# Optimization experiments

Hardware: AMD Instinct MI355X
Metric: run time of the kernel (lower is better)

The kernel has to match this reference:

```python
import jax, jax.numpy as jnp
from jax import lax
import numpy as np

# Shapes / hyperparams (match init_kwargs and input_specs)
B, C1, H1, W1 = 4, 128, 128, 128      # x1: low-level feature map
C2, H2, W2 = 64, 64, 64               # x2: high-level feature map (H1 = rate*H2)
KSIZE, STRIDE, RATE, SIZE = 3, 1, 2, 2
KERNEL = SIZE * RATE                  # 4 = raw patch size
SCALE = 10.0
GROUPS, OUT_C = 4, 64
RATES = (1, 2, 4, 8)
L = H2 * W2                           # number of patches / attention bins


def extract_patches(x, k, s):
    """torch extract_patches: zero-pad (k-1)//2, unfold -> [B, L, C, k, k]."""
    pad = (k - 1) // 2 if k != 1 else 0
    p = lax.conv_general_dilated_patches(x, (k, k), (s, s), [(pad, pad), (pad, pad)])
    Bn, Ckk, oH, oW = p.shape
    C = Ckk // (k * k)
    p = p.reshape(Bn, C, k, k, oH, oW)
    return jnp.transpose(p, (0, 4, 5, 1, 2, 3)).reshape(Bn, oH * oW, C, k, k)


def setup_inputs():
    key = jax.random.key(0)
    ks = jax.random.split(key, 5)
    x1 = jax.random.normal(ks[0], (B, C1, H1, W1), jnp.float32)
    x2 = jax.random.normal(ks[1], (B, C2, H2, W2), jnp.float32)
    # mask: 1 indicates holes; central square hole at x1 resolution
    mask = jnp.zeros((B, 1, H1, W1), jnp.float32)
    mask = mask.at[:, :, H1 // 4:3 * H1 // 4, W1 // 4:3 * W1 // 4].set(1.0)
    mask_all = jax.random.uniform(ks[2], (B, 1, H2, W2), jnp.float32)
    conv_w = jax.random.normal(ks[3], (GROUPS, OUT_C // GROUPS, C1, 3, 3), jnp.float32) * 0.05
    conv_b = jax.random.normal(ks[4], (GROUPS, OUT_C // GROUPS), jnp.float32) * 0.01
    return {"x1": x1, "x2": x2, "mask": mask, "mask_all": mask_all,
            "conv_w": conv_w, "conv_b": conv_b}


def reference(x1, x2, mask, mask_all, conv_w, conv_b):
    raw_w = extract_patches(x1, KERNEL, RATE * STRIDE)   # [B, L, C1, 4, 4] value patches
    w = extract_patches(x2, KSIZE, STRIDE)               # [B, L, C2, 3, 3] key patches
    # F.interpolate(mask, size=x1 HW, align_corners=True) is identity (mask already H1xW1)
    m = extract_patches(mask, KERNEL, 2).mean(axis=(2, 3, 4))   # [B, L]
    mm = (m == 0.0).astype(x1.dtype)                            # 1 = fully valid patch
    # F.interpolate(mask_all, size=x2 HW) is identity (already H2xW2)

    pad_s = (KSIZE - 1) // 2
    pad_t = KERNEL - 1 - (KERNEL - 1) // 2  # conv_transpose2d(padding=(KERNEL-1)//2)

    def attend(xi, wi, raw_wi, mi, ma):
        # xi [C2,H2,W2], wi [L,C2,3,3], raw_wi [L,C1,4,4], mi [L], ma [1,H2,W2]
        norm = jnp.sqrt(jnp.sum(wi * wi, axis=(1, 2, 3), keepdims=True))
        wn = wi / jnp.maximum(norm, 1e-4)
        # correlation scores: conv2d(xi, normalized key patches) -> [L, H2, W2]
        yi = lax.conv_general_dilated(
            xi[None], wn, (1, 1), [(pad_s, pad_s)] * 2,
            dimension_numbers=('NCHW', 'OIHW', 'NCHW'))[0]
        mi3 = mi[:, None, None]
        yi = yi * mi3 * ma
        yi = jax.nn.softmax(yi * SCALE, axis=0)
        yi = jnp.maximum(yi * mi3 * ma, 1e-8)
        # value aggregation: conv_transpose2d(yi, raw_wi, stride=RATE, padding=1)
        out = lax.conv_general_dilated(
            yi[None], raw_wi[:, :, ::-1, ::-1], (1, 1), [(pad_t, pad_t)] * 2,
            lhs_dilation=(RATE, RATE),
            dimension_numbers=('NCHW', 'IOHW', 'NCHW'))[0]
        return out / float(KERNEL)                        # [C1, H1, W1]

    y = jax.vmap(attend)(x2, w, raw_w, mm, mask_all)      # [B, C1, H1, W1]

    # fuse: GROUPS dilated 3x3 conv + ReLU branches, concatenated on channels
    outs = []
    for i in range(GROUPS):
        r = RATES[i]
        o = lax.conv_general_dilated(
            y, conv_w[i], (1, 1), [(r, r)] * 2, rhs_dilation=(r, r),
            dimension_numbers=('NCHW', 'OIHW', 'NCHW'))
        outs.append(jax.nn.relu(o + conv_b[i][None, :, None, None]))
    return jnp.concatenate(outs, axis=1)                  # [B, OUT_C, H1, W1]
```

## Files before the change

### kernel.cpp

```cpp
#include <hip/hip_runtime.h>
#include <math.h>

typedef _Float16 f16;
typedef __attribute__((ext_vector_type(8))) _Float16 f16x8;
typedef __attribute__((ext_vector_type(4))) float f32x4;
typedef __attribute__((ext_vector_type(16))) float f32x16;

#define LPOS 4096
#define KPAT 576
#define RPAT 2048
#define PPAD 20736
#define ROWS 18432

#define GLDS(g, l) __builtin_amdgcn_global_load_lds( \
    (const __attribute__((address_space(1))) void*)(g), \
    (__attribute__((address_space(3))) void*)(l), 16, 0, 0)

__global__ __launch_bounds__(64) void build_P_norm(const float* __restrict__ x2b,
                                                   f16* __restrict__ Ph,
                                                   float* __restrict__ rnorm) {
    int pos = blockIdx.x;
    int u = pos >> 6, v = pos & 63;
    int tid = threadIdx.x;
    float ss = 0.f;
    for (int k = tid; k < KPAT; k += 64) {
        int c = k / 9, r9 = k % 9;
        int di = r9 / 3, dj = r9 % 3;
        int yy = u + di - 1, xx = v + dj - 1;
        float val = 0.f;
        if (yy >= 0 && yy < 64 && xx >= 0 && xx < 64)
            val = x2b[c * 4096 + yy * 64 + xx];
        Ph[pos * KPAT + k] = (f16)val;
        ss += val * val;
    }
#pragma unroll
    for (int off = 32; off; off >>= 1) ss += __shfl_xor(ss, off, 64);
    if (tid == 0) rnorm[pos] = 1.f / fmaxf(sqrtf(ss), 1e-4f);
}

__global__ __launch_bounds__(256) void compact_mask_all(const float* __restrict__ mask,
                                                        int* __restrict__ cidx_all,
                                                        int* __restrict__ nk_all) {
    int b = blockIdx.x;
    const float* maskb = mask + (size_t)b * 16384;
    int* cidx = cidx_all + b * 4352;
    int* nk = nk_all + b * 2;
    int tid = threadIdx.x;
    int keep[16];
    int cnt = 0;
#pragma unroll
    for (int e = 0; e < 16; ++e) {
        int pos = tid * 16 + e;
        int pu = pos >> 6, pv = pos & 63;
        float s = 0.f;
        for (int t = 0; t < 4; ++t)
            for (int w = 0; w < 4; ++w) {
                int yy = 2 * pu - 1 + t, xx = 2 * pv - 1 + w;
                if (yy >= 0 && yy < 128 && xx >= 0 && xx < 128)
                    s += maskb[yy * 128 + xx];
            }
        keep[e] = (s == 0.f) ? 1 : 0;
        cnt += keep[e];
    }
    __shared__ int ps[256];
    ps[tid] = cnt;
    __syncthreads();
    for (int off = 1; off < 256; off <<= 1) {
        int v = (tid >= off) ? ps[tid - off] : 0;
        __syncthreads();
        ps[tid] += v;
        __syncthreads();
    }
    int total = ps[255];
    int base = ps[tid] - cnt;
#pragma unroll
    for (int e = 0; e < 16; ++e)
        if (keep[e]) cidx[base++] = tid * 16 + e;
    for (int i = total + tid; i < 4352; i += 256) cidx[i] = 0;
    if (tid == 0) { nk[0] = total; nk[1] = (total + 63) & ~63; }
}

__global__ __launch_bounds__(256) void zero_halo(f16* __restrict__ ybTp) {
    int idx = blockIdx.x * 256 + threadIdx.x;
    int b = idx / 331776; if (b >= 4) return;
    int rem = idx % 331776;
    int q = rem & 15, pos = rem >> 4;
    int yy = pos / 144, xx = pos % 144;
    if (yy >= 8 && yy < 136 && xx >= 8 && xx < 136) return;
    *(f16x8*)(ybTp + (size_t)b * PPAD * 128 + (size_t)yy * ROWS + q * 1152 + xx * 8) = (f16x8){};
}

__global__ __launch_bounds__(256) void gemm_score_mfma(const f16* __restrict__ Ph,
                                                       const int* __restrict__ cidx,
                                                       const float* __restrict__ rnorm,
                                                       const int* __restrict__ nk,
                                                       f16* __restrict__ S) {
    int n0 = blockIdx.x * 128;
    if (n0 >= nk[0]) return;
    __shared__ f16 Ash[128 * 32], Bsh[128 * 32];
    int tid = threadIdx.x;
    int w = tid >> 6, lane = tid & 63;
    int wy = w >> 1, wx = w & 1;
    int m0 = blockIdx.y * 128;
    f32x16 acc[2][2];
#pragma unroll
    for (int mt = 0; mt < 2; ++mt)
#pragma unroll
        for (int nt = 0; nt < 2; ++nt)
#pragma unroll
            for (int e = 0; e < 16; ++e) acc[mt][nt][e] = 0.f;
    int srow = lane >> 2;
    int cblk = lane & 3;
    int scol = (cblk ^ ((srow >> 1) & 3)) * 8;
    int dcol = cblk * 8;
    int l31 = lane & 31, kh2 = lane >> 5;
    int arow[2], brow[2], asw[2], bsw[2];
#pragma unroll
    for (int i = 0; i < 2; ++i) {
        arow[i] = wy * 64 + i * 32 + l31;
        brow[i] = wx * 64 + i * 32 + l31;
        asw[i] = (arow[i] >> 1) & 3;
        bsw[i] = (brow[i] >> 1) & 3;
    }
    const f16* Asrc[2]; const f16* Bsrc[2]; int ldso[2];
#pragma unroll
    for (int i = 0; i < 2; ++i) {
        int row = w * 32 + i * 16 + srow;
        ldso[i] = row * 32 + dcol;
        Asrc[i] = Ph + (size_t)(m0 + row) * KPAT + scol;
        Bsrc[i] = Ph + (size_t)cidx[n0 + row] * KPAT + scol;
    }
    for (int k0 = 0; k0 < KPAT; k0 += 32) {
#pragma unroll
        for (int i = 0; i < 2; ++i) {
            GLDS(Asrc[i] + k0, Ash + ldso[i]);
            GLDS(Bsrc[i] + k0, Bsh + ldso[i]);
        }
        __syncthreads();
#pragma unroll
        for (int kh = 0; kh < 2; ++kh) {
            int blk = kh * 2 + kh2;
            f16x8 va[2], vb[2];
#pragma unroll
            for (int i = 0; i < 2; ++i) {
                va[i] = *(const f16x8*)&Ash[arow[i] * 32 + ((blk ^ asw[i]) * 8)];
                vb[i] = *(const f16x8*)&Bsh[brow[i] * 32 + ((blk ^ bsw[i]) * 8)];
            }
#pragma unroll
            for (int mt = 0; mt < 2; ++mt)
#pragma unroll
                for (int nt = 0; nt < 2; ++nt)
                    acc[mt][nt] = __builtin_amdgcn_mfma_f32_32x32x16_f16(va[mt], vb[nt], acc[mt][nt], 0, 0, 0);
        }
        __syncthreads();
    }
    int rbase = 4 * kh2;
#pragma unroll
    for (int mt = 0; mt < 2; ++mt)
#pragma unroll
        for (int nt = 0; nt < 2; ++nt) {
            int col = n0 + wx * 64 + nt * 32 + l31;
            float rn = rnorm[cidx[col]];
#pragma unroll
            for (int rg = 0; rg < 16; ++rg) {
                int row = m0 + wy * 64 + mt * 32 + (rg & 3) + 8 * (rg >> 2) + rbase;
                S[(size_t)row * LPOS + col] = (f16)(acc[mt][nt][rg] * rn);
            }
        }
}

__global__ __launch_bounds__(256) void softmax_mask(const f16* __restrict__ S,
                                                    const int* __restrict__ nk,
                                                    const float* __restrict__ mab,
                                                    f16* __restrict__ Ah) {
    int pos = blockIdx.x;
    int tid = threadIdx.x;
    int nkeep = nk[0], kpad = nk[1];
    float ma = mab[pos];
    float sc = 10.0f * ma;
    const f16* Srow = S + (size_t)pos * LPOS;
    float v[16];
    float vmax = (nkeep < LPOS) ? 0.f : -3.0e38f;
#pragma unroll
    for (int i = 0; i < 2; ++i) {
        int jb = (tid + i * 256) * 8;
        f16x8 x8 = *(const f16x8*)(Srow + jb);
#pragma unroll
        for (int e = 0; e < 8; ++e) {
            float x = (jb + e < nkeep) ? (float)x8[e] * sc : -3.0e38f;
            v[i * 8 + e] = x;
            vmax = fmaxf(vmax, x);
        }
    }
#pragma unroll
    for (int off = 32; off; off >>= 1) vmax = fmaxf(vmax, __shfl_xor(vmax, off, 64));
    __shared__ float sred[4];
    int wid = tid >> 6;
    if ((tid & 63) == 0) sred[wid] = vmax;
    __syncthreads();
    vmax = fmaxf(fmaxf(sred[0], sred[1]), fmaxf(sred[2], sred[3]));
    __syncthreads();
    float ssum = 0.f;
#pragma unroll
    for (int i = 0; i < 16; ++i) {
        float e = (v[i] > -1.0e37f) ? __expf(v[i] - vmax) : 0.f;
        v[i] = e;
        ssum += e;
    }
#pragma unroll
    for (int off = 32; off; off >>= 1) ssum += __shfl_xor(ssum, off, 64);
    if ((tid & 63) == 0) sred[wid] = ssum;
    __syncthreads();
    float total = sred[0] + sred[1] + sred[2] + sred[3]
                + (float)(LPOS - nkeep) * __expf(-vmax);
    float inv = 1.f / total;
#pragma unroll
    for (int i = 0; i < 2; ++i) {
        int jb = (tid + i * 256) * 8;
        if (jb >= kpad) continue;
        f16x8 h;
#pragma unroll
        for (int e = 0; e < 8; ++e)
            h[e] = (jb + e < nkeep) ? (f16)(v[i * 8 + e] * inv * ma) : (f16)0.f;
        *(f16x8*)(Ah + (size_t)pos * LPOS + jb) = h;
    }
}

__global__ __launch_bounds__(256) void build_Rt(const float* __restrict__ x1b,
                                                const int* __restrict__ cidx,
                                                const int* __restrict__ nk,
                                                f16* __restrict__ Rt) {
    int idx = blockIdx.x * 256 + threadIdx.x;
    int j = idx & 4095, n = idx >> 12;
    if (j >= nk[1]) return;
    int p = cidx[j];
    int pu = p >> 6, pv = p & 63;
    int t = (n >> 9) & 3, s = (n >> 7) & 3, c = n & 127;
    int yy = 2 * pu - 1 + t, xx = 2 * pv - 1 + s;
    float val = 0.f;
    if (yy >= 0 && yy < 128 && xx >= 0 && xx < 128)
        val = x1b[c * 16384 + yy * 128 + xx];
    Rt[idx] = (f16)val;
}

__global__ __launch_bounds__(256) void gemm_deconv_mfma(const f16* __restrict__ A,
                                                        const f16* __restrict__ Bt,
                                                        const int* __restrict__ nk,
                                                        f16* __restrict__ V) {
    __shared__ f16 Ash[128 * 64], Bsh[128 * 64];
    int kpad = nk[1];
    int id = blockIdx.x;
    int m0 = ((id & 7) * 4 + ((id >> 3) & 3)) * 128;
    int n0 = (id >> 5) * 128;
    int tid = threadIdx.x;
    int w = tid >> 6, lane = tid & 63;
    int wy = w >> 1, wx = w & 1;
    f32x16 acc[2][2];
#pragma unroll
    for (int mt = 0; mt < 2; ++mt)
#pragma unroll
        for (int nt = 0; nt < 2; ++nt)
#pragma unroll
            for (int e = 0; e < 16; ++e) acc[mt][nt][e] = 0.f;
    int srow = lane >> 3;
    int cblk = lane & 7;
    int scol = (cblk ^ srow) * 8;
    int l31 = lane & 31, kh2 = lane >> 5;
    int f7 = l31 & 7;
    int arow[2], brow[2];
#pragma unroll
    for (int i = 0; i < 2; ++i) {
        arow[i] = wy * 64 + i * 32 + l31;
        brow[i] = wx * 64 + i * 32 + l31;
    }
    for (int k0 = 0; k0 < kpad; k0 += 64) {
#pragma unroll
        for (int i = 0; i < 4; ++i) {
            int row = w * 32 + i * 8 + srow;
            int ldso = row * 64 + cblk * 8;
            GLDS(A + (size_t)(m0 + row) * LPOS + k0 + scol, Ash + ldso);
            GLDS(Bt + (size_t)(n0 + row) * LPOS + k0 + scol, Bsh + ldso);
        }
        __syncthreads();
#pragma unroll
        for (int kh = 0; kh < 4; ++kh) {
            int slot = (kh * 2 + kh2) ^ f7;
            f16x8 va[2], vb[2];
#pragma unroll
            for (int i = 0; i < 2; ++i) {
                va[i] = *(const f16x8*)&Ash[arow[i] * 64 + slot * 8];
                vb[i] = *(const f16x8*)&Bsh[brow[i] * 64 + slot * 8];
            }
#pragma unroll
            for (int mt = 0; mt < 2; ++mt)
#pragma unroll
                for (int nt = 0; nt < 2; ++nt)
                    acc[mt][nt] = __builtin_amdgcn_mfma_f32_32x32x16_f16(va[mt], vb[nt], acc[mt][nt], 0, 0, 0);
        }
        __syncthreads();
    }
    int rbase = 4 * kh2;
#pragma unroll
    for (int mt = 0; mt < 2; ++mt)
#pragma unroll
        for (int nt = 0; nt < 2; ++nt) {
            int col = n0 + wx * 64 + nt * 32 + l31;
#pragma unroll
            for (int rg = 0; rg < 16; ++rg) {
                int row = m0 + wy * 64 + mt * 32 + (rg & 3) + 8 * (rg >> 2) + rbase;
                V[(size_t)row * RPAT + col] = (f16)acc[mt][nt][rg];
            }
        }
}

__global__ __launch_bounds__(256) void reconstruct(const f16* __restrict__ V,
                                                   f16* __restrict__ ybTpb) {
    int idx = blockIdx.x * 256 + threadIdx.x;
    int c = idx & 127, p = idx >> 7;
    int xx = p & 127, yy = p >> 7;
    float sum = 0.f;
    int tby = (yy & 1) ? 0 : 1;
    int tbx = (xx & 1) ? 0 : 1;
#pragma unroll
    for (int dt = 0; dt < 2; ++dt) {
        int t = tby + 2 * dt;
        int u2 = yy + 1 - t;
        if (u2 < 0 || u2 >= 128) continue;
        int u = u2 >> 1;
#pragma unroll
        for (int ds = 0; ds < 2; ++ds) {
            int s = tbx + 2 * ds;
            int v2 = xx + 1 - s;
            if (v2 < 0 || v2 >= 128) continue;
            int v = v2 >> 1;
            sum += (float)V[(size_t)(u * 64 + v) * RPAT + (t * 4 + s) * 128 + c];
        }
    }
    ybTpb[(size_t)(yy + 8) * ROWS + (c >> 3) * 1152 + (xx + 8) * 8 + (c & 7)] = (f16)(0.25f * sum);
}

__global__ __launch_bounds__(256) void prep_w(const float* __restrict__ cw,
                                              f16* __restrict__ Wt) {
    int idx = blockIdx.x * 256 + threadIdx.x;
    if (idx >= 4 * 9 * 16 * 128) return;
    int g = idx / 18432, rem = idx % 18432;
    int tap = rem >> 11, oc = (rem >> 7) & 15, c = rem & 127;
    Wt[idx] = (f16)cw[(((g * 16 + oc) * 128 + c) * 9) + tap];
}

__global__ __launch_bounds__(256) void final_conv_mfma(const f16* __restrict__ ybTp,
                                                       const f16* __restrict__ Wt,
                                                       const float* __restrict__ cb,
                                                       float* __restrict__ out) {
    int id = blockIdx.x;
    int p = id & 7;
    int b = p >> 1, yhalf = p & 1;
    int rest = id >> 3;
    int g = rest >> 6;
    int y = yhalf * 64 + (rest & 63);
    int tid = threadIdx.x, w = tid >> 6, lane = tid & 63;
    int xbase = w * 32;
    int r = 1 << g;
    int m = lane & 15, q = lane >> 4;
    const f16* yB = ybTp + (size_t)b * PPAD * 128;
    const f16* Wg = Wt + g * 18432 + m * 128 + q * 8;
    f32x4 acc[2];
    acc[0] = (f32x4){0.f, 0.f, 0.f, 0.f};
    acc[1] = (f32x4){0.f, 0.f, 0.f, 0.f};
#pragma unroll
    for (int tap = 0; tap < 9; ++tap) {
        int dy = (tap / 3 - 1) * r, dx = (tap % 3 - 1) * r;
        const f16* rowb = yB + (size_t)(y + dy + 8) * ROWS + q * 1152
                        + (xbase + m + 8 + dx) * 8;
        const f16* wrow = Wg + tap * 2048;
#pragma unroll
        for (int ks = 0; ks < 4; ++ks) {
            f16x8 bfrag = *(const f16x8*)(wrow + ks * 32);
            f16x8 a0 = *(const f16x8*)(rowb + ks * 4608);
            f16x8 a1 = *(const f16x8*)(rowb + ks * 4608 + 128);
            acc[0] = __builtin_amdgcn_mfma_f32_16x16x32_f16(a0, bfrag, acc[0], 0, 0, 0);
            acc[1] = __builtin_amdgcn_mfma_f32_16x16x32_f16(a1, bfrag, acc[1], 0, 0, 0);
        }
    }
    float bias = cb[g * 16 + m];
    float* orow = out + ((size_t)(b * 64 + g * 16 + m)) * 16384 + (size_t)y * 128;
#pragma unroll
    for (int mt = 0; mt < 2; ++mt)
#pragma unroll
        for (int ri = 0; ri < 4; ++ri) {
            int x = xbase + mt * 16 + q * 4 + ri;
            orow[x] = fmaxf(acc[mt][ri] + bias, 0.f);
        }
}

extern "C" void kernel_launch(void* const* d_in, const int* in_sizes, int n_in,
                              void* d_out, int out_size, void* d_ws, size_t ws_size,
                              hipStream_t stream) {
    const float* x1 = (const float*)d_in[0];
    const float* x2 = (const float*)d_in[1];
    const float* mask = (const float*)d_in[2];
    const float* mask_all = (const float*)d_in[3];
    const float* conv_w = (const float*)d_in[4];
    const float* conv_b = (const float*)d_in[5];
    float* out = (float*)d_out;

    char* ws = (char*)d_ws;
    f16*   Ph    = (f16*)  (ws + 0);
    float* rnorm = (float*)(ws + 4718592);
    int*   cidx  = (int*)  (ws + 4734976);
    int*   nk    = (int*)  (ws + 4804608);
    f16*   S     = (f16*)  (ws + 9469952);
    f16*   V     = (f16*)  (ws + 43024384);
    f16*   Ah    = (f16*)  (ws + 76578816);
    f16*   Rt    = (f16*)  (ws + 110133248);
    f16*   ybTp  = (f16*)  (ws + 126910464);
    f16*   Wt    = (f16*)  (ws + 148144128);

    prep_w<<<288, 256, 0, stream>>>(conv_w, Wt);
    compact_mask_all<<<4, 256, 0, stream>>>(mask, cidx, nk);
    zero_halo<<<5184, 256, 0, stream>>>(ybTp);
    for (int b = 0; b < 4; ++b) {
        const float* x2b = x2 + (size_t)b * 64 * 4096;
        const float* x1b = x1 + (size_t)b * 128 * 16384;
        const int* cb_idx = cidx + b * 4352;
        const int* nkb = nk + b * 2;
        build_P_norm<<<4096, 64, 0, stream>>>(x2b, Ph, rnorm);
        gemm_score_mfma<<<dim3(32, 32), 256, 0, stream>>>(Ph, cb_idx, rnorm, nkb, S);
        softmax_mask<<<4096, 256, 0, stream>>>(S, nkb, mask_all + (size_t)b * 4096, Ah);
        build_Rt<<<32768, 256, 0, stream>>>(x1b, cb_idx, nkb, Rt);
        gemm_deconv_mfma<<<512, 256, 0, stream>>>(Ah, Rt, nkb, V);
        reconstruct<<<8192, 256, 0, stream>>>(V, ybTp + (size_t)b * PPAD * 128);
    }
    final_conv_mfma<<<2048, 256, 0, stream>>>(ybTp, Wt, conv_b, out);
}
```

Before: 676.0 us.

## Batch deconv GEMM across all images with 256x256 tiles and LDS pipelining

Adds a new gemm_deconv8 kernel that runs the value-aggregation GEMM for all four batch images in one launch. It uses 512-thread blocks, 256x256 output tiles, 16x16x32 MFMAs, double-buffered global-to-LDS loads and an XCD-aware block remap. Per-batch Ah/Rt/V buffers are laid out separately so the GEMM no longer serialises with the per-batch loop, and the padded K is rounded to 128 to fit the two-tile inner step. This needs a much larger workspace, and the old path is kept as a fallback when ws_size is too small.

```diff
diff --git a/kernel.cpp b/kernel.cpp
--- a/kernel.cpp
+++ b/kernel.cpp
@@ -77,7 +77,7 @@
     for (int e = 0; e < 16; ++e)
         if (keep[e]) cidx[base++] = tid * 16 + e;
     for (int i = total + tid; i < 4352; i += 256) cidx[i] = 0;
-    if (tid == 0) { nk[0] = total; nk[1] = (total + 63) & ~63; }
+    if (tid == 0) { nk[0] = total; nk[1] = (total + 127) & ~127; }
 }
 
 __global__ __launch_bounds__(256) void zero_halo(f16* __restrict__ ybTp) {
@@ -311,6 +311,141 @@
                 V[(size_t)row * RPAT + col] = (f16)acc[mt][nt][rg];
             }
         }
+}
+
+__global__ __launch_bounds__(512, 2) void gemm_deconv8(const f16* __restrict__ Ah4,
+                                                       const f16* __restrict__ Rt4,
+                                                       const int* __restrict__ nk_all,
+                                                       f16* __restrict__ V4) {
+    __shared__ __align__(16) f16 L[65536];
+    int id = blockIdx.x;
+    int orig = (id & 7) * 64 + (id >> 3);
+    int b = orig >> 7;
+    int t = orig & 127;
+    int m0 = (t >> 3) * 256, n0 = (t & 7) * 256;
+    const f16* Ag = Ah4 + (size_t)b * 4096 * 4096;
+    const f16* Bg = Rt4 + (size_t)b * 2048 * 4096;
+    f16* V = V4 + (size_t)b * 4096 * 2048;
+    int kpad2 = nk_all[b * 2 + 1];
+    int ntile = kpad2 >> 6;
+    int NI = ntile >> 1;
+
+    int tid = threadIdx.x;
+    int lane = tid & 63, wid = tid >> 6;
+    int wy = wid >> 2, wx = wid & 3;
+    int r16 = lane & 15, q = lane >> 4;
+
+    int sr = tid >> 3, sc = tid & 7;
+    int colo = (sc ^ ((sr >> 1) & 2)) * 8;
+    const f16* pA = Ag + (size_t)(m0 + sr) * 4096 + colo;
+    const f16* pB = Bg + (size_t)(n0 + sr) * 4096 + colo;
+    f16* ldsT = L + tid * 8;
+
+    int s2 = (r16 >> 1) & 2;
+    const f16* aBase = L + (wy * 128 + r16) * 64 + (q ^ s2) * 8;
+    const f16* bBase = L + 16384 + (wx * 64 + r16) * 64 + (q ^ s2) * 8;
+
+    f32x4 acc[8][4];
+#pragma unroll
+    for (int i = 0; i < 8; ++i)
+#pragma unroll
+        for (int j = 0; j < 4; ++j) acc[i][j] = (f32x4){0.f, 0.f, 0.f, 0.f};
+
+    f16x8 af[4][2], b0[2][2], bc[2][2];
+
+#define STG64(bf, isB, h, g, kt) do { \
+    int kk_ = ((kt) < ntile) ? (kt) * 64 : 0; \
+    const f16* s_ = ((isB) ? pB : pA) + (size_t)((h) * 128 + (g) * 64) * 4096 + kk_; \
+    GLDS(s_, ldsT + (bf) * 32768 + (isB) * 16384 + ((h) * 128 + (g) * 64) * 64); \
+} while (0)
+#define STGH(bf, isB, h, kt) do { STG64(bf, isB, h, 0, kt); STG64(bf, isB, h, 1, kt); } while (0)
+#define RDA(bf, msub) do { \
+    _Pragma("unroll") for (int mf_ = 0; mf_ < 4; ++mf_) \
+    _Pragma("unroll") for (int ks_ = 0; ks_ < 2; ++ks_) \
+        af[mf_][ks_] = *(const f16x8*)(aBase + (bf) * 32768 + (msub) * 4096 + mf_ * 1024 + ks_ * 32); \
+} while (0)
+#define RDB(dst, bf, nsub) do { \
+    _Pragma("unroll") for (int nf_ = 0; nf_ < 2; ++nf_) \
+    _Pragma("unroll") for (int ks_ = 0; ks_ < 2; ++ks_) \
+        dst[nf_][ks_] = *(const f16x8*)(bBase + (bf) * 32768 + (nsub) * 2048 + nf_ * 1024 + ks_ * 32); \
+} while (0)
+#define QMM(msub, nsub, bfr) do { \
+    __builtin_amdgcn_s_setprio(1); \
+    _Pragma("unroll") for (int mf_ = 0; mf_ < 4; ++mf_) \
+    _Pragma("unroll") for (int nf_ = 0; nf_ < 2; ++nf_) \
+    _Pragma("unroll") for (int ks_ = 0; ks_ < 2; ++ks_) \
+        acc[(msub) * 4 + mf_][(nsub) * 2 + nf_] = __builtin_amdgcn_mfma_f32_16x16x32_f16( \
+            af[mf_][ks_], bfr[nf_][ks_], acc[(msub) * 4 + mf_][(nsub) * 2 + nf_], 0, 0, 0); \
+    __builtin_amdgcn_s_setprio(0); \
+} while (0)
+#define BAR()  __builtin_amdgcn_s_barrier()
+#define VMW4() asm volatile("s_waitcnt vmcnt(4)" ::: "memory")
+
+    STGH(0, 1, 0, 0); STGH(0, 1, 1, 0);
+    STGH(0, 0, 0, 0); STGH(0, 0, 1, 0);
+    STGH(1, 1, 0, 1); STGH(1, 1, 1, 1);
+    VMW4(); BAR();
+
+    for (int i = 0; i < NI; ++i) {
+        int kt1 = 2 * i + 1, kt2 = 2 * i + 2, kt3 = 2 * i + 3;
+        RDA(0, 0); RDB(b0, 0, 0);
+        STGH(1, 0, 0, kt1);
+        BAR();
+        QMM(0, 0, b0);
+        BAR();
+        RDB(bc, 0, 1);
+        STGH(1, 0, 1, kt1);
+        BAR();
+        QMM(0, 1, bc);
+        BAR();
+        RDA(0, 1);
+        STGH(0, 1, 0, kt2);
+        BAR();
+        QMM(1, 1, bc);
+        BAR();
+        STGH(0, 1, 1, kt2);
+        BAR();
+        QMM(1, 0, b0);
+        VMW4(); BAR();
+        RDA(1, 0); RDB(b0, 1, 0);
+        STGH(0, 0, 0, kt2);
+        BAR();
+        QMM(0, 0, b0);
+        BAR();
+        RDB(bc, 1, 1);
+        STGH(0, 0, 1, kt2);
+        BAR();
+        QMM(0, 1, bc);
+        BAR();
+        RDA(1, 1);
+        STGH(1, 1, 0, kt3);
+        BAR();
+        QMM(1, 1, bc);
+        BAR();
+        STGH(1, 1, 1, kt3);
+        BAR();
+        QMM(1, 0, b0);
+        VMW4(); BAR();
+    }
+
+#pragma unroll
+    for (int mf8 = 0; mf8 < 8; ++mf8) {
+        int row = m0 + wy * 128 + mf8 * 16 + q * 4;
+#pragma unroll
+        for (int nf = 0; nf < 4; ++nf) {
+            int col = n0 + wx * 64 + nf * 16 + r16;
+#pragma unroll
+            for (int g = 0; g < 4; ++g)
+                V[(size_t)(row + g) * RPAT + col] = (f16)acc[mf8][nf][g];
+        }
+    }
+#undef STG64
+#undef STGH
+#undef RDA
+#undef RDB
+#undef QMM
+#undef BAR
+#undef VMW4
 }
 
 __global__ __launch_bounds__(256) void reconstruct(const f16* __restrict__ V,
@@ -405,31 +540,66 @@
     float* out = (float*)d_out;
 
     char* ws = (char*)d_ws;
-    f16*   Ph    = (f16*)  (ws + 0);
-    float* rnorm = (float*)(ws + 4718592);
-    int*   cidx  = (int*)  (ws + 4734976);
-    int*   nk    = (int*)  (ws + 4804608);
-    f16*   S     = (f16*)  (ws + 9469952);
-    f16*   V     = (f16*)  (ws + 43024384);
-    f16*   Ah    = (f16*)  (ws + 76578816);
-    f16*   Rt    = (f16*)  (ws + 110133248);
-    f16*   ybTp  = (f16*)  (ws + 126910464);
-    f16*   Wt    = (f16*)  (ws + 148144128);
-
-    prep_w<<<288, 256, 0, stream>>>(conv_w, Wt);
-    compact_mask_all<<<4, 256, 0, stream>>>(mask, cidx, nk);
-    zero_halo<<<5184, 256, 0, stream>>>(ybTp);
-    for (int b = 0; b < 4; ++b) {
-        const float* x2b = x2 + (size_t)b * 64 * 4096;
-        const float* x1b = x1 + (size_t)b * 128 * 16384;
-        const int* cb_idx = cidx + b * 4352;
-        const int* nkb = nk + b * 2;
-        build_P_norm<<<4096, 64, 0, stream>>>(x2b, Ph, rnorm);
-        gemm_score_mfma<<<dim3(32, 32), 256, 0, stream>>>(Ph, cb_idx, rnorm, nkb, S);
-        softmax_mask<<<4096, 256, 0, stream>>>(S, nkb, mask_all + (size_t)b * 4096, Ah);
-        build_Rt<<<32768, 256, 0, stream>>>(x1b, cb_idx, nkb, Rt);
-        gemm_deconv_mfma<<<512, 256, 0, stream>>>(Ah, Rt, nkb, V);
-        reconstruct<<<8192, 256, 0, stream>>>(V, ybTp + (size_t)b * PPAD * 128);
-    }
-    final_conv_mfma<<<2048, 256, 0, stream>>>(ybTp, Wt, conv_b, out);
-}
+    const size_t NEED_BATCHED = 328102144ull;
+
+    if (ws_size >= NEED_BATCHED) {
+        f16*   Ph    = (f16*)  (ws + 0);
+        float* rnorm = (float*)(ws + 4718592);
+        int*   cidx  = (int*)  (ws + 4734976);
+        int*   nk    = (int*)  (ws + 4804608);
+        f16*   Wt    = (f16*)  (ws + 4804864);
+        f16*   S     = (f16*)  (ws + 4878592);
+        f16*   ybTp  = (f16*)  (ws + 38433024);
+        f16*   Ah    = (f16*)  (ws + 59666688);
+        f16*   Rt    = (f16*)  (ws + 193884416);
+        f16*   V     = (f16*)  (ws + 260993280);
+
+        prep_w<<<288, 256, 0, stream>>>(conv_w, Wt);
+        compact_mask_all<<<4, 256, 0, stream>>>(mask, cidx, nk);
+        zero_halo<<<5184, 256, 0, stream>>>(ybTp);
+        for (int b = 0; b < 4; ++b) {
+            const float* x2b = x2 + (size_t)b * 64 * 4096;
+            const float* x1b = x1 + (size_t)b * 128 * 16384;
+            const int* cb_idx = cidx + b * 4352;
+            const int* nkb = nk + b * 2;
+            build_P_norm<<<4096, 64, 0, stream>>>(x2b, Ph, rnorm);
+            gemm_score_mfma<<<dim3(32, 32), 256, 0, stream>>>(Ph, cb_idx, rnorm, nkb, S);
+            softmax_mask<<<4096, 256, 0, stream>>>(S, nkb, mask_all + (size_t)b * 4096,
+                                                   Ah + (size_t)b * 16777216);
+            build_Rt<<<32768, 256, 0, stream>>>(x1b, cb_idx, nkb, Rt + (size_t)b * 8388608);
+        }
+        gemm_deconv8<<<512, 512, 0, stream>>>(Ah, Rt, nk, V);
+        for (int b = 0; b < 4; ++b)
+            reconstruct<<<8192, 256, 0, stream>>>(V + (size_t)b * 8388608,
+                                                  ybTp + (size_t)b * PPAD * 128);
+        final_conv_mfma<<<2048, 256, 0, stream>>>(ybTp, Wt, conv_b, out);
+    } else {
+        f16*   Ph    = (f16*)  (ws + 0);
+        float* rnorm = (float*)(ws + 4718592);
+        int*   cidx  = (int*)  (ws + 4734976);
+        int*   nk    = (int*)  (ws + 4804608);
+        f16*   S     = (f16*)  (ws + 9469952);
+        f16*   V     = (f16*)  (ws + 43024384);
+        f16*   Ah    = (f16*)  (ws + 76578816);
+        f16*   Rt    = (f16*)  (ws + 110133248);
+        f16*   ybTp  = (f16*)  (ws + 126910464);
+        f16*   Wt    = (f16*)  (ws + 148144128);
+
+        prep_w<<<288, 256, 0, stream>>>(conv_w, Wt);
+        compact_mask_all<<<4, 256, 0, stream>>>(mask, cidx, nk);
+        zero_halo<<<5184, 256, 0, stream>>>(ybTp);
+        for (int b = 0; b < 4; ++b) {
+            const float* x2b = x2 + (size_t)b * 64 * 4096;
+            const float* x1b = x1 + (size_t)b * 128 * 16384;
+            const int* cb_idx = cidx + b * 4352;
+            const int* nkb = nk + b * 2;
+            build_P_norm<<<4096, 64, 0, stream>>>(x2b, Ph, rnorm);
+            gemm_score_mfma<<<dim3(32, 32), 256, 0, stream>>>(Ph, cb_idx, rnorm, nkb, S);
+            softmax_mask<<<4096, 256, 0, stream>>>(S, nkb, mask_all + (size_t)b * 4096, Ah);
+            build_Rt<<<32768, 256, 0, stream>>>(x1b, cb_idx, nkb, Rt);
+            gemm_deconv_mfma<<<512, 256, 0, stream>>>(Ah, Rt, nkb, V);
+            reconstruct<<<8192, 256, 0, stream>>>(V, ybTp + (size_t)b * PPAD * 128);
+        }
+        final_conv_mfma<<<2048, 256, 0, stream>>>(ybTp, Wt, conv_b, out);
+    }
+}
```

New measurement: 675.2 us. No clear change (-0.1%).

## Rewrite deconv GEMM with 256x128 tiles and double-buffered interleaved LDS pipeline

Applied to the files above, without the earlier changes.

Replaces the 128x128 single-buffered deconv GEMM with a 512-thread kernel using 256x128 output tiles. It keeps two LDS buffers and interleaves global-to-LDS prefetch of the next K tiles with 16x16x32 MFMA sub-blocks, raising wave priority around the MFMAs. The goal is to hide global load latency and the barrier stalls of the old load-sync-compute loop. The K padding is rounded to 128 so each loop iteration covers two 64-wide tiles. In exchange the kernel uses more LDS and more barriers per iteration, and its hand-placed waitcnt counts are fragile. The extra padding also adds some zero work in the other kernels that read the padded count.

```diff
diff --git a/kernel.cpp b/kernel.cpp
--- a/kernel.cpp
+++ b/kernel.cpp
@@ -77,7 +77,7 @@
     for (int e = 0; e < 16; ++e)
         if (keep[e]) cidx[base++] = tid * 16 + e;
     for (int i = total + tid; i < 4352; i += 256) cidx[i] = 0;
-    if (tid == 0) { nk[0] = total; nk[1] = (total + 63) & ~63; }
+    if (tid == 0) { nk[0] = total; nk[1] = (total + 127) & ~127; }
 }
 
 __global__ __launch_bounds__(256) void zero_halo(f16* __restrict__ ybTp) {
@@ -243,74 +243,124 @@
     Rt[idx] = (f16)val;
 }
 
-__global__ __launch_bounds__(256) void gemm_deconv_mfma(const f16* __restrict__ A,
-                                                        const f16* __restrict__ Bt,
-                                                        const int* __restrict__ nk,
-                                                        f16* __restrict__ V) {
-    __shared__ f16 Ash[128 * 64], Bsh[128 * 64];
+__global__ __launch_bounds__(512, 2) void gemm_deconv2(const f16* __restrict__ A,
+                                                       const f16* __restrict__ Bt,
+                                                       const int* __restrict__ nk,
+                                                       f16* __restrict__ V) {
+    __shared__ __align__(16) f16 L[49152];
+    int id = blockIdx.x;
+    int orig = (id & 7) * 32 + (id >> 3);
+    int mt = orig >> 4, nt = orig & 15;
+    int m0 = mt * 256, n0 = nt * 128;
     int kpad = nk[1];
-    int id = blockIdx.x;
-    int m0 = ((id & 7) * 4 + ((id >> 3) & 3)) * 128;
-    int n0 = (id >> 5) * 128;
+    int ntile = kpad >> 6;
+    int NI = ntile >> 1;
+
     int tid = threadIdx.x;
-    int w = tid >> 6, lane = tid & 63;
-    int wy = w >> 1, wx = w & 1;
-    f32x16 acc[2][2];
-#pragma unroll
-    for (int mt = 0; mt < 2; ++mt)
-#pragma unroll
-        for (int nt = 0; nt < 2; ++nt)
-#pragma unroll
-            for (int e = 0; e < 16; ++e) acc[mt][nt][e] = 0.f;
-    int srow = lane >> 3;
-    int cblk = lane & 7;
-    int scol = (cblk ^ srow) * 8;
-    int l31 = lane & 31, kh2 = lane >> 5;
-    int f7 = l31 & 7;
-    int arow[2], brow[2];
-#pragma unroll
-    for (int i = 0; i < 2; ++i) {
-        arow[i] = wy * 64 + i * 32 + l31;
-        brow[i] = wx * 64 + i * 32 + l31;
-    }
-    for (int k0 = 0; k0 < kpad; k0 += 64) {
-#pragma unroll
-        for (int i = 0; i < 4; ++i) {
-            int row = w * 32 + i * 8 + srow;
-            int ldso = row * 64 + cblk * 8;
-            GLDS(A + (size_t)(m0 + row) * LPOS + k0 + scol, Ash + ldso);
-            GLDS(Bt + (size_t)(n0 + row) * LPOS + k0 + scol, Bsh + ldso);
-        }
-        __syncthreads();
-#pragma unroll
-        for (int kh = 0; kh < 4; ++kh) {
-            int slot = (kh * 2 + kh2) ^ f7;
-            f16x8 va[2], vb[2];
-#pragma unroll
-            for (int i = 0; i < 2; ++i) {
-                va[i] = *(const f16x8*)&Ash[arow[i] * 64 + slot * 8];
-                vb[i] = *(const f16x8*)&Bsh[brow[i] * 64 + slot * 8];
-            }
-#pragma unroll
-            for (int mt = 0; mt < 2; ++mt)
-#pragma unroll
-                for (int nt = 0; nt < 2; ++nt)
-                    acc[mt][nt] = __builtin_amdgcn_mfma_f32_32x32x16_f16(va[mt], vb[nt], acc[mt][nt], 0, 0, 0);
-        }
-        __syncthreads();
-    }
-    int rbase = 4 * kh2;
-#pragma unroll
-    for (int mt = 0; mt < 2; ++mt)
-#pragma unroll
-        for (int nt = 0; nt < 2; ++nt) {
-            int col = n0 + wx * 64 + nt * 32 + l31;
-#pragma unroll
-            for (int rg = 0; rg < 16; ++rg) {
-                int row = m0 + wy * 64 + mt * 32 + (rg & 3) + 8 * (rg >> 2) + rbase;
-                V[(size_t)row * RPAT + col] = (f16)acc[mt][nt][rg];
-            }
-        }
+    int lane = tid & 63, wid = tid >> 6;
+    int wy = wid >> 1, wx = wid & 1;
+    int r16 = lane & 15, q = lane >> 4;
+
+    int sr = tid >> 3, sc = tid & 7;
+    int colo = (sc ^ (sr & 7)) * 8;
+    const f16* pA = A  + (size_t)(m0 + sr) * 4096 + colo;
+    const f16* pB = Bt + (size_t)(n0 + sr) * 4096 + colo;
+
+    int s3 = r16 & 7;
+    int qs = (q ^ (s3 & 3)) * 8;
+    int kf = s3 >> 2;
+    const f16* aB = L + (wy * 64 + r16) * 64 + qs;
+    const f16* bB = L + 16384 + (wx * 64 + r16) * 64 + qs;
+
+    f32x4 acc[4][4];
+#pragma unroll
+    for (int i = 0; i < 4; ++i)
+#pragma unroll
+        for (int j = 0; j < 4; ++j) acc[i][j] = (f32x4){0.f, 0.f, 0.f, 0.f};
+
+    f16x8 af[2][2], b0[2][2], bc[2][2];
+
+#define STGA(bf, u, kt) do { \
+    int kk_ = ((kt) < ntile) ? (kt) * 64 : 0; \
+    GLDS(pA + (size_t)(u) * 262144 + kk_, L + (bf) * 24576 + (u) * 4096 + tid * 8); \
+} while (0)
+#define STGB(bf, u, kt) do { \
+    int kk_ = ((kt) < ntile) ? (kt) * 64 : 0; \
+    GLDS(pB + (size_t)(u) * 262144 + kk_, L + (bf) * 24576 + 16384 + (u) * 4096 + tid * 8); \
+} while (0)
+#define RDA(bf, msub) do { \
+    _Pragma("unroll") for (int mf_ = 0; mf_ < 2; ++mf_) \
+    _Pragma("unroll") for (int ks_ = 0; ks_ < 2; ++ks_) \
+        af[mf_][ks_] = *(const f16x8*)(aB + (bf) * 24576 + (msub) * 2048 + mf_ * 1024 + ((ks_ ^ kf) << 5)); \
+} while (0)
+#define RDB(dst, bf, nsub) do { \
+    _Pragma("unroll") for (int nf_ = 0; nf_ < 2; ++nf_) \
+    _Pragma("unroll") for (int ks_ = 0; ks_ < 2; ++ks_) \
+        dst[nf_][ks_] = *(const f16x8*)(bB + (bf) * 24576 + (nsub) * 2048 + nf_ * 1024 + ((ks_ ^ kf) << 5)); \
+} while (0)
+#define QMM(msub, nsub, bfr) do { \
+    __builtin_amdgcn_s_setprio(1); \
+    _Pragma("unroll") for (int mf_ = 0; mf_ < 2; ++mf_) \
+    _Pragma("unroll") for (int nf_ = 0; nf_ < 2; ++nf_) \
+    _Pragma("unroll") for (int ks_ = 0; ks_ < 2; ++ks_) \
+        acc[(msub) * 2 + mf_][(nsub) * 2 + nf_] = __builtin_amdgcn_mfma_f32_16x16x32_f16( \
+            af[mf_][ks_], bfr[nf_][ks_], acc[(msub) * 2 + mf_][(nsub) * 2 + nf_], 0, 0, 0); \
+    __builtin_amdgcn_s_setprio(0); \
+} while (0)
+#define BAR()  __builtin_amdgcn_s_barrier()
+#define VMW2() asm volatile("s_waitcnt vmcnt(2)" ::: "memory")
+
+    STGB(0, 0, 0); STGB(0, 1, 0);
+    STGA(0, 0, 0); STGA(0, 1, 0); STGA(0, 2, 0); STGA(0, 3, 0);
+    STGB(1, 0, 1); STGB(1, 1, 1);
+    VMW2(); BAR();
+
+    for (int i = 0; i < NI; ++i) {
+        int kt1 = 2 * i + 1, kt2 = 2 * i + 2, kt3 = 2 * i + 3;
+        RDA(0, 0); RDB(b0, 0, 0);
+        STGA(1, 0, kt1); STGA(1, 1, kt1);
+        BAR(); QMM(0, 0, b0); BAR();
+        RDB(bc, 0, 1);
+        STGA(1, 2, kt1); STGA(1, 3, kt1);
+        BAR(); QMM(0, 1, bc); BAR();
+        RDA(0, 1);
+        STGB(0, 0, kt2); STGB(0, 1, kt2);
+        BAR(); QMM(1, 1, bc); BAR();
+        QMM(1, 0, b0);
+        VMW2(); BAR();
+        RDA(1, 0); RDB(b0, 1, 0);
+        STGA(0, 0, kt2); STGA(0, 1, kt2);
+        BAR(); QMM(0, 0, b0); BAR();
+        RDB(bc, 1, 1);
+        STGA(0, 2, kt2); STGA(0, 3, kt2);
+        BAR(); QMM(0, 1, bc); BAR();
+        RDA(1, 1);
+        STGB(1, 0, kt3); STGB(1, 1, kt3);
+        BAR(); QMM(1, 1, bc); BAR();
+        QMM(1, 0, b0);
+        VMW2(); BAR();
+    }
+
+    asm volatile("s_waitcnt vmcnt(0)" ::: "memory");
+
+#pragma unroll
+    for (int mi = 0; mi < 4; ++mi) {
+        int row = m0 + wy * 64 + mi * 16 + q * 4;
+#pragma unroll
+        for (int ni = 0; ni < 4; ++ni) {
+            int col = n0 + wx * 64 + ni * 16 + r16;
+#pragma unroll
+            for (int g = 0; g < 4; ++g)
+                V[(size_t)(row + g) * RPAT + col] = (f16)acc[mi][ni][g];
+        }
+    }
+#undef STGA
+#undef STGB
+#undef RDA
+#undef RDB
+#undef QMM
+#undef BAR
+#undef VMW2
 }
 
 __global__ __launch_bounds__(256) void reconstruct(const f16* __restrict__ V,
@@ -428,7 +478,7 @@
         gemm_score_mfma<<<dim3(32, 32), 256, 0, stream>>>(Ph, cb_idx, rnorm, nkb, S);
         softmax_mask<<<4096, 256, 0, stream>>>(S, nkb, mask_all + (size_t)b * 4096, Ah);
         build_Rt<<<32768, 256, 0, stream>>>(x1b, cb_idx, nkb, Rt);
-        gemm_deconv_mfma<<<512, 256, 0, stream>>>(Ah, Rt, nkb, V);
+        gemm_deconv2<<<256, 512, 0, stream>>>(Ah, Rt, nkb, V);
         reconstruct<<<8192, 256, 0, stream>>>(V, ybTp + (size_t)b * PPAD * 128);
     }
     final_conv_mfma<<<2048, 256, 0, stream>>>(ybTp, Wt, conv_b, out);
```

Result: faster. 624.9 us (-7.6%).
